# Optimization experiments

Measured on AMD Instinct MI355X. Metric: run time of the kernel, lower is better.

## Reference

```python
import jax, jax.numpy as jnp
import numpy as np

EMBED, HEADS, LEVELS, POINTS = 256, 8, 1, 4


def setup_inputs():
    key = jax.random.key(0)
    ks = jax.random.split(key, 8)
    B, NQ = 8, 8192
    Hh, Ww = 128, 128
    E, Hn, L, P = EMBED, HEADS, LEVELS, POINTS
    s = 1.0 / np.sqrt(E)
    return dict(
        query=jax.random.normal(ks[0], (B, NQ, E), jnp.float32),
        value=jax.random.normal(ks[1], (B, Hh * Ww, E), jnp.float32),
        ref_2d=jax.random.uniform(ks[2], (B, NQ, L, 2), dtype=jnp.float32),
        spatial_shapes=jnp.array([[Hh, Ww]], dtype=jnp.int32),
        W_off=jax.random.normal(ks[3], (E, Hn * L * P * 2), jnp.float32) * 0.01,
        b_off=jax.random.normal(ks[4], (Hn * L * P * 2,), jnp.float32) * 0.5,
        W_attn=jax.random.normal(ks[5], (E, Hn * L * P), jnp.float32) * s,
        b_attn=jnp.zeros((Hn * L * P,), jnp.float32),
        W_val=jax.random.normal(ks[6], (E, E), jnp.float32) * s,
        b_val=jnp.zeros((E,), jnp.float32),
        W_out=jax.random.normal(ks[7], (E, E), jnp.float32) * s,
        b_out=jnp.zeros((E,), jnp.float32),
    )


def _bilinear_sample(v, loc, Hl, Wl):
    # v: (B, Hn, Hl*Wl, dh); loc: (B, Hn, NQ, P, 2) normalized [0,1] (x, y)
    B, Hn, NQ, P, _ = loc.shape
    dh = v.shape[-1]
    # torch grid_sample(align_corners=False) pixel coords: p = loc * size - 0.5
    x = loc[..., 0] * Wl - 0.5
    y = loc[..., 1] * Hl - 0.5
    x0 = jnp.floor(x); y0 = jnp.floor(y)
    x1 = x0 + 1.0; y1 = y0 + 1.0
    wx1 = x - x0; wx0 = 1.0 - wx1
    wy1 = y - y0; wy0 = 1.0 - wy1

    def corner(xc, yc, w):
        valid = (xc >= 0) & (xc < Wl) & (yc >= 0) & (yc < Hl)  # zeros padding
        xi = jnp.clip(xc, 0, Wl - 1).astype(jnp.int32)
        yi = jnp.clip(yc, 0, Hl - 1).astype(jnp.int32)
        idx = (yi * Wl + xi).reshape(B, Hn, NQ * P, 1)
        vals = jnp.take_along_axis(v, idx, axis=2).reshape(B, Hn, NQ, P, dh)
        return vals * (w * valid.astype(v.dtype))[..., None]

    return (corner(x0, y0, wx0 * wy0) + corner(x1, y0, wx1 * wy0)
            + corner(x0, y1, wx0 * wy1) + corner(x1, y1, wx1 * wy1))


def _forward(query, value, ref_2d, W_off, b_off, W_attn, b_attn, W_val, b_val, W_out, b_out, shapes):
    B, NQ, E = query.shape
    Hn, L, P = HEADS, LEVELS, POINTS
    dh = E // Hn
    NV = value.shape[1]
    identity = query
    v = (value @ W_val + b_val).reshape(B, NV, Hn, dh)
    off = (query @ W_off + b_off).reshape(B, NQ, Hn, L, P, 2)
    attn = jax.nn.softmax((query @ W_attn + b_attn).reshape(B, NQ, Hn, L * P), axis=-1)
    attn = attn.reshape(B, NQ, Hn, L, P)
    # offset_normalizer = (W, H) per level
    norm = jnp.asarray(shapes[:, ::-1].copy(), dtype=query.dtype)
    loc = ref_2d[:, :, None, :, None, :] + off / norm[None, None, None, :, None, :]
    loc = jnp.transpose(loc, (0, 2, 1, 3, 4, 5))   # (B, Hn, NQ, L, P, 2)
    attn_t = jnp.transpose(attn, (0, 2, 1, 3, 4))  # (B, Hn, NQ, L, P)
    v_t = jnp.transpose(v, (0, 2, 1, 3))           # (B, Hn, NV, dh)
    starts = np.concatenate([[0], np.cumsum(shapes[:, 0] * shapes[:, 1])]).astype(np.int64)
    out = jnp.zeros((B, Hn, NQ, dh), query.dtype)
    for l in range(L):  # static small loop over feature levels
        Hl, Wl = int(shapes[l, 0]), int(shapes[l, 1])
        v_l = v_t[:, :, int(starts[l]):int(starts[l + 1]), :]
        samp = _bilinear_sample(v_l, loc[:, :, :, l], Hl, Wl)  # (B,Hn,NQ,P,dh)
        out = out + jnp.sum(samp * attn_t[:, :, :, l, :, None], axis=3)
    out = jnp.transpose(out, (0, 2, 1, 3)).reshape(B, NQ, E)
    # dropout is identity at eval time
    return out @ W_out + b_out + identity


def reference(query, value, ref_2d, spatial_shapes, W_off, b_off, W_attn, b_attn, W_val, b_val, W_out, b_out):
    shapes = np.asarray(jax.device_get(spatial_shapes))  # static level shapes
    return _forward(query, value, ref_2d, W_off, b_off, W_attn, b_attn, W_val, b_val, W_out, b_out, shapes)
```

## Files before the change

### kernel.cpp

```cpp
#include <hip/hip_runtime.h>

typedef short s16x8 __attribute__((ext_vector_type(8)));
typedef float f32x4 __attribute__((ext_vector_type(4)));

#define HN 8
#define PP 4
#define DH 32
#define NQc 8192
#define NVc 16384
#define EE 256
#define HWc 128

__device__ __forceinline__ unsigned short f2bf(float x) {
  unsigned u = __float_as_uint(x);
  u += 0x7FFF + ((u >> 16) & 1);
  return (unsigned short)(u >> 16);
}
__device__ __forceinline__ float bf2f(unsigned short h) {
  return __uint_as_float(((unsigned)h) << 16);
}

__global__ __launch_bounds__(256) void wprep(
    const float* __restrict__ Wval, const float* __restrict__ Wout,
    const float* __restrict__ Woff, const float* __restrict__ Wattn,
    const float* __restrict__ boff, const float* __restrict__ battn,
    unsigned short* __restrict__ wvt, unsigned short* __restrict__ wot,
    unsigned short* __restrict__ wct, float* __restrict__ bcat) {
  int g = blockIdx.x * 256 + threadIdx.x;
  if (g < 65536) {
    int n = g >> 8, k = g & 255;
    wvt[n * 256 + k] = f2bf(Wval[k * 256 + n]);
  } else if (g < 131072) {
    int g2 = g - 65536;
    int n = g2 >> 8, k = g2 & 255;
    wot[n * 256 + k] = f2bf(Wout[k * 256 + n]);
  } else if (g < 163840) {
    int g2 = g - 131072;
    int n = g2 >> 8, k = g2 & 255;
    float v = 0.f;
    if (n < 64) v = Woff[k * 64 + n];
    else if (n < 96) v = Wattn[k * 32 + (n - 64)];
    wct[n * 256 + k] = f2bf(v);
  } else if (g < 163968) {
    int c = g - 163840;
    bcat[c] = (c < 64) ? boff[c] : ((c < 96) ? battn[c - 64] : 0.f);
  }
}

#define MODE_VAL 0
#define MODE_PLAIN 1
#define MODE_OUT 2

template <int MODE>
struct SmemBytes { static constexpr int v = 20480; };
template <> struct SmemBytes<MODE_PLAIN> { static constexpr int v = 51200; };

template <int MODE, bool ABF16>
__global__ __launch_bounds__(256) void mfma_gemm(
    const void* __restrict__ Ain, const unsigned short* __restrict__ Wt,
    const float* __restrict__ bias, const float* __restrict__ resid,
    const float* __restrict__ ref2d, unsigned int* __restrict__ meta,
    void* __restrict__ outp) {
  __shared__ __align__(16) char smem[SmemBytes<MODE>::v];
  unsigned short* As = (unsigned short*)smem;
  unsigned short* Ws = As + 128 * 40;
  const int t = threadIdx.x;
  const int lane = t & 63, wave = t >> 6;
  const int lane15 = lane & 15, quad = lane >> 4;
  const int wr = wave >> 1, wc = wave & 1;
  const int bm = blockIdx.x * 128, bn = blockIdx.y * 128;

  f32x4 acc[4][4];
#pragma unroll
  for (int i = 0; i < 4; ++i)
#pragma unroll
    for (int j = 0; j < 4; ++j)
#pragma unroll
      for (int r = 0; r < 4; ++r) acc[i][j][r] = 0.f;

  const int ar = t >> 3, ac = (t & 7) * 4;
  const int wr2 = t >> 1, wcp = (t & 1) * 2;

  float4 av[4];
  uint4 ab0, ab1, wv0, wv1;

#define LOAD_TILE(K0)                                                          \
  do {                                                                         \
    if (!ABF16) {                                                              \
      const float* Af = (const float*)Ain;                                     \
      _Pragma("unroll") for (int i = 0; i < 4; ++i)                            \
          av[i] = *(const float4*)(Af + (size_t)(bm + ar + i * 32) * 256 +     \
                                   (K0) + ac);                                 \
    } else {                                                                   \
      const unsigned short* Ab = (const unsigned short*)Ain;                   \
      ab0 = *(const uint4*)(Ab + (size_t)(bm + wr2) * 256 + (K0) + wcp * 8);   \
      ab1 = *(const uint4*)(Ab + (size_t)(bm + wr2) * 256 + (K0) + wcp * 8 + 8); \
    }                                                                          \
    wv0 = *(const uint4*)(Wt + (size_t)(bn + wr2) * 256 + (K0) + wcp * 8);     \
    wv1 = *(const uint4*)(Wt + (size_t)(bn + wr2) * 256 + (K0) + wcp * 8 + 8); \
  } while (0)

  LOAD_TILE(0);

  for (int k0 = 0; k0 < 256; k0 += 32) {
    __syncthreads();
    if (!ABF16) {
#pragma unroll
      for (int i = 0; i < 4; ++i) {
        ushort4 c;
        c.x = f2bf(av[i].x); c.y = f2bf(av[i].y); c.z = f2bf(av[i].z); c.w = f2bf(av[i].w);
        *(ushort4*)&As[(ar + i * 32) * 40 + ac] = c;
      }
    } else {
      *(uint4*)&As[wr2 * 40 + wcp * 8] = ab0;
      *(uint4*)&As[wr2 * 40 + wcp * 8 + 8] = ab1;
    }
    *(uint4*)&Ws[wr2 * 40 + wcp * 8] = wv0;
    *(uint4*)&Ws[wr2 * 40 + wcp * 8 + 8] = wv1;
    __syncthreads();
    if (k0 < 224) LOAD_TILE(k0 + 32);
    s16x8 af[4], bfr[4];
#pragma unroll
    for (int tm = 0; tm < 4; ++tm)
      af[tm] = *(const s16x8*)&As[(wr * 64 + tm * 16 + lane15) * 40 + quad * 8];
#pragma unroll
    for (int tn = 0; tn < 4; ++tn)
      bfr[tn] = *(const s16x8*)&Ws[(wc * 64 + tn * 16 + lane15) * 40 + quad * 8];
#pragma unroll
    for (int tm = 0; tm < 4; ++tm)
#pragma unroll
      for (int tn = 0; tn < 4; ++tn)
        acc[tm][tn] = __builtin_amdgcn_mfma_f32_16x16x32_bf16(bfr[tn], af[tm], acc[tm][tn], 0, 0, 0);
  }
#undef LOAD_TILE

  if (MODE == MODE_VAL) {
    unsigned short* outs = (unsigned short*)outp;
    const size_t b = (size_t)(bm >> 14);
    const int n0 = bm & (NVc - 1);
#pragma unroll
    for (int tn = 0; tn < 4; ++tn) {
      const int ch0 = bn + wc * 64 + tn * 16 + quad * 4;
      const float4 b4 = *(const float4*)&bias[ch0];
      const int h = ch0 >> 5, dh0 = ch0 & 31;
#pragma unroll
      for (int tm = 0; tm < 4; ++tm) {
        const int n = n0 + wr * 64 + tm * 16 + lane15;
        ushort4 o;
        o.x = f2bf(acc[tm][tn][0] + b4.x);
        o.y = f2bf(acc[tm][tn][1] + b4.y);
        o.z = f2bf(acc[tm][tn][2] + b4.z);
        o.w = f2bf(acc[tm][tn][3] + b4.w);
        *(ushort4*)(outs + ((b * HN + h) * NVc + n) * DH + dh0) = o;
      }
    }
  } else if (MODE == MODE_PLAIN) {
    float* Cf = (float*)smem;
    __syncthreads();
#pragma unroll
    for (int tn = 0; tn < 4; ++tn) {
      const int col0 = wc * 64 + tn * 16 + quad * 4;
      if (col0 < 96) {
        const float4 b4 = *(const float4*)&bias[col0];
#pragma unroll
        for (int tm = 0; tm < 4; ++tm) {
          const int m = wr * 64 + tm * 16 + lane15;
          float4 v;
          v.x = acc[tm][tn][0] + b4.x;
          v.y = acc[tm][tn][1] + b4.y;
          v.z = acc[tm][tn][2] + b4.z;
          v.w = acc[tm][tn][3] + b4.w;
          *(float4*)&Cf[m * 100 + col0] = v;
        }
      }
    }
    __syncthreads();
#pragma unroll
    for (int i = 0; i < 4; ++i) {
      const int task = i * 256 + t;
      const int h = task & 7, rowl = task >> 3;
      const int bq = bm + rowl;
      const float* row = Cf + rowl * 100;
      const float rx = ref2d[(size_t)bq * 2 + 0];
      const float ry = ref2d[(size_t)bq * 2 + 1];
      const float l0 = row[64 + h * 4 + 0], l1 = row[64 + h * 4 + 1];
      const float l2 = row[64 + h * 4 + 2], l3 = row[64 + h * 4 + 3];
      const float mx = fmaxf(fmaxf(l0, l1), fmaxf(l2, l3));
      float e0 = __expf(l0 - mx), e1 = __expf(l1 - mx), e2 = __expf(l2 - mx), e3 = __expf(l3 - mx);
      const float inv = 1.0f / (e0 + e1 + e2 + e3);
      float ee[4] = {e0, e1, e2, e3};
      unsigned int* m = meta + ((size_t)bq * 8 + h) * 20;
      uint4 pk;
      float4 wts[4];
#pragma unroll
      for (int p = 0; p < PP; ++p) {
        const float a = ee[p] * inv;
        const float ox = row[h * 8 + p * 2 + 0];
        const float oy = row[h * 8 + p * 2 + 1];
        const float x = (rx + ox * (1.0f / HWc)) * (float)HWc - 0.5f;
        const float y = (ry + oy * (1.0f / HWc)) * (float)HWc - 0.5f;
        const float x0f = floorf(x), y0f = floorf(y);
        const int x0 = (int)x0f, y0 = (int)y0f;
        const float wx1 = x - x0f, wx0 = 1.f - wx1;
        const float wy1 = y - y0f, wy0 = 1.f - wy1;
        const bool vx0 = (unsigned)x0 < (unsigned)HWc, vx1 = (unsigned)(x0 + 1) < (unsigned)HWc;
        const bool vy0 = (unsigned)y0 < (unsigned)HWc, vy1 = (unsigned)(y0 + 1) < (unsigned)HWc;
        const int xi0 = min(max(x0, 0), HWc - 1), xi1 = min(max(x0 + 1, 0), HWc - 1);
        const int yi0 = min(max(y0, 0), HWc - 1), yi1 = min(max(y0 + 1, 0), HWc - 1);
        const unsigned pv = (unsigned)xi0 | ((unsigned)yi0 << 8) | ((unsigned)xi1 << 16) | ((unsigned)yi1 << 24);
        if (p == 0) pk.x = pv; else if (p == 1) pk.y = pv; else if (p == 2) pk.z = pv; else pk.w = pv;
        float4 w;
        w.x = (vx0 && vy0) ? a * wx0 * wy0 : 0.f;
        w.y = (vx1 && vy0) ? a * wx1 * wy0 : 0.f;
        w.z = (vx0 && vy1) ? a * wx0 * wy1 : 0.f;
        w.w = (vx1 && vy1) ? a * wx1 * wy1 : 0.f;
        wts[p] = w;
      }
      *(uint4*)m = pk;
#pragma unroll
      for (int p = 0; p < PP; ++p) *(float4*)&m[4 + p * 4] = wts[p];
    }
  } else {
    float* outf = (float*)outp;
#pragma unroll
    for (int tn = 0; tn < 4; ++tn) {
      const int ch0 = bn + wc * 64 + tn * 16 + quad * 4;
      const float4 b4 = *(const float4*)&bias[ch0];
#pragma unroll
      for (int tm = 0; tm < 4; ++tm) {
        const size_t row = (size_t)bm + wr * 64 + tm * 16 + lane15;
        float4 rs = *(const float4*)(resid + row * 256 + ch0);
        float4 v;
        v.x = acc[tm][tn][0] + b4.x + rs.x;
        v.y = acc[tm][tn][1] + b4.y + rs.y;
        v.z = acc[tm][tn][2] + b4.z + rs.z;
        v.w = acc[tm][tn][3] + b4.w + rs.w;
        *(float4*)(outf + row * 256 + ch0) = v;
      }
    }
  }
}

__global__ __launch_bounds__(256) void sample_kernel(
    const unsigned short* __restrict__ vbuf,
    const unsigned int* __restrict__ meta,
    unsigned short* __restrict__ outs) {
  const int t = threadIdx.x;
  const int d4 = (t & 7) << 2;
  const int ql = t >> 3;
  const int sl = blockIdx.x >> 8;
  const int qc = blockIdx.x & 255;
  const int b = sl >> 3;
  const int h = sl & 7;
  const int q = qc * 32 + ql;
  const size_t bq = (size_t)b * NQc + q;
  const unsigned int* m = meta + ((size_t)bq * 8 + h) * 20;
  const uint4 pk = *(const uint4*)m;
  const unsigned short* vb = vbuf + (size_t)sl * (NVc * DH) + d4;

  float4 acc = {0.f, 0.f, 0.f, 0.f};
#pragma unroll
  for (int p = 0; p < PP; ++p) {
    const unsigned P = (p == 0) ? pk.x : (p == 1) ? pk.y : (p == 2) ? pk.z : pk.w;
    const float4 w = *(const float4*)(m + 4 + p * 4);
    const int x0 = P & 255, y0 = (P >> 8) & 255, x1 = (P >> 16) & 255, y1 = P >> 24;
    const int r0 = y0 << 12, r1 = y1 << 12;
    const ushort4 v00 = *(const ushort4*)(vb + r0 + (x0 << 5));
    const ushort4 v10 = *(const ushort4*)(vb + r0 + (x1 << 5));
    const ushort4 v01 = *(const ushort4*)(vb + r1 + (x0 << 5));
    const ushort4 v11 = *(const ushort4*)(vb + r1 + (x1 << 5));
    acc.x += w.x * bf2f(v00.x); acc.y += w.x * bf2f(v00.y);
    acc.z += w.x * bf2f(v00.z); acc.w += w.x * bf2f(v00.w);
    acc.x += w.y * bf2f(v10.x); acc.y += w.y * bf2f(v10.y);
    acc.z += w.y * bf2f(v10.z); acc.w += w.y * bf2f(v10.w);
    acc.x += w.z * bf2f(v01.x); acc.y += w.z * bf2f(v01.y);
    acc.z += w.z * bf2f(v01.z); acc.w += w.z * bf2f(v01.w);
    acc.x += w.w * bf2f(v11.x); acc.y += w.w * bf2f(v11.y);
    acc.z += w.w * bf2f(v11.z); acc.w += w.w * bf2f(v11.w);
  }
  ushort4 o;
  o.x = f2bf(acc.x); o.y = f2bf(acc.y); o.z = f2bf(acc.z); o.w = f2bf(acc.w);
  *(ushort4*)(outs + bq * EE + h * DH + d4) = o;
}

extern "C" void kernel_launch(void* const* d_in, const int* in_sizes, int n_in,
                              void* d_out, int out_size, void* d_ws, size_t ws_size,
                              hipStream_t stream) {
  const float* query = (const float*)d_in[0];
  const float* value = (const float*)d_in[1];
  const float* ref2d = (const float*)d_in[2];
  const float* Woff  = (const float*)d_in[4];
  const float* boff  = (const float*)d_in[5];
  const float* Wattn = (const float*)d_in[6];
  const float* battn = (const float*)d_in[7];
  const float* Wval  = (const float*)d_in[8];
  const float* bval  = (const float*)d_in[9];
  const float* Wout  = (const float*)d_in[10];
  const float* bout  = (const float*)d_in[11];
  float* out = (float*)d_out;

  unsigned short* vbuf = (unsigned short*)d_ws;
  unsigned int* meta   = (unsigned int*)(vbuf + 33554432);
  unsigned short* sbuf = (unsigned short*)(meta + 10485760);
  unsigned short* wvt  = sbuf + 16777216;
  unsigned short* wot  = wvt + 65536;
  unsigned short* wct  = wot + 65536;
  float* bcat          = (float*)(wct + 32768);

  wprep<<<641, 256, 0, stream>>>(Wval, Wout, Woff, Wattn, boff, battn, wvt, wot, wct, bcat);

  mfma_gemm<MODE_VAL, false><<<dim3(1024, 2), 256, 0, stream>>>(
      (const void*)value, wvt, bval, nullptr, nullptr, nullptr, (void*)vbuf);

  mfma_gemm<MODE_PLAIN, false><<<dim3(512, 1), 256, 0, stream>>>(
      (const void*)query, wct, bcat, nullptr, ref2d, meta, nullptr);

  sample_kernel<<<16384, 256, 0, stream>>>(vbuf, meta, sbuf);

  mfma_gemm<MODE_OUT, true><<<dim3(512, 2), 256, 0, stream>>>(
      (const void*)sbuf, wot, bout, query, nullptr, nullptr, (void*)out);
}
```

Measured before the change: 424.0 us.

## Double-buffer GEMM shared-memory tiles and coalesce output epilogue through LDS

The GEMM main loop now uses two shared-memory tile buffers, so each iteration needs one barrier instead of two and the next tile's LDS store overlaps with the current tile's MFMA work. The fp32 output epilogue (MODE_OUT/PLAIN) now stages accumulators through LDS in two half-tile passes, giving row-contiguous, coalesced residual reads and output writes. This doubles LDS use for the VAL/OUT variants, which may lower occupancy, and adds extra barriers in the epilogue.

Result: no change. 426.0 us (+0.5%).

```diff
diff --git a/kernel.cpp b/kernel.cpp
--- a/kernel.cpp
+++ b/kernel.cpp
@@ -52,7 +52,7 @@
 #define MODE_OUT 2
 
 template <int MODE>
-struct SmemBytes { static constexpr int v = 20480; };
+struct SmemBytes { static constexpr int v = 40960; };
 template <> struct SmemBytes<MODE_PLAIN> { static constexpr int v = 51200; };
 
 template <int MODE, bool ABF16>
@@ -62,8 +62,10 @@
     const float* __restrict__ ref2d, unsigned int* __restrict__ meta,
     void* __restrict__ outp) {
   __shared__ __align__(16) char smem[SmemBytes<MODE>::v];
-  unsigned short* As = (unsigned short*)smem;
-  unsigned short* Ws = As + 128 * 40;
+  unsigned short* As0 = (unsigned short*)smem;
+  unsigned short* Ws0 = As0 + 128 * 40;
+  unsigned short* As1 = Ws0 + 128 * 40;
+  unsigned short* Ws1 = As1 + 128 * 40;
   const int t = threadIdx.x;
   const int lane = t & 63, wave = t >> 6;
   const int lane15 = lane & 15, quad = lane >> 4;
@@ -100,39 +102,53 @@
     wv1 = *(const uint4*)(Wt + (size_t)(bn + wr2) * 256 + (K0) + wcp * 8 + 8); \
   } while (0)
 
+#define STAGE(AsD, WsD)                                                        \
+  do {                                                                         \
+    if (!ABF16) {                                                              \
+      _Pragma("unroll") for (int i = 0; i < 4; ++i) {                          \
+        ushort4 c;                                                             \
+        c.x = f2bf(av[i].x); c.y = f2bf(av[i].y);                              \
+        c.z = f2bf(av[i].z); c.w = f2bf(av[i].w);                              \
+        *(ushort4*)&(AsD)[(ar + i * 32) * 40 + ac] = c;                        \
+      }                                                                        \
+    } else {                                                                   \
+      *(uint4*)&(AsD)[wr2 * 40 + wcp * 8] = ab0;                               \
+      *(uint4*)&(AsD)[wr2 * 40 + wcp * 8 + 8] = ab1;                           \
+    }                                                                          \
+    *(uint4*)&(WsD)[wr2 * 40 + wcp * 8] = wv0;                                 \
+    *(uint4*)&(WsD)[wr2 * 40 + wcp * 8 + 8] = wv1;                             \
+  } while (0)
+
   LOAD_TILE(0);
-
-  for (int k0 = 0; k0 < 256; k0 += 32) {
-    __syncthreads();
-    if (!ABF16) {
-#pragma unroll
-      for (int i = 0; i < 4; ++i) {
-        ushort4 c;
-        c.x = f2bf(av[i].x); c.y = f2bf(av[i].y); c.z = f2bf(av[i].z); c.w = f2bf(av[i].w);
-        *(ushort4*)&As[(ar + i * 32) * 40 + ac] = c;
-      }
-    } else {
-      *(uint4*)&As[wr2 * 40 + wcp * 8] = ab0;
-      *(uint4*)&As[wr2 * 40 + wcp * 8 + 8] = ab1;
-    }
-    *(uint4*)&Ws[wr2 * 40 + wcp * 8] = wv0;
-    *(uint4*)&Ws[wr2 * 40 + wcp * 8 + 8] = wv1;
-    __syncthreads();
-    if (k0 < 224) LOAD_TILE(k0 + 32);
+  STAGE(As0, Ws0);
+  __syncthreads();
+
+#pragma unroll
+  for (int kk = 0; kk < 8; ++kk) {
+    unsigned short* Ar = (kk & 1) ? As1 : As0;
+    unsigned short* Wr = (kk & 1) ? Ws1 : Ws0;
+    if (kk < 7) LOAD_TILE((kk + 1) * 32);
     s16x8 af[4], bfr[4];
 #pragma unroll
     for (int tm = 0; tm < 4; ++tm)
-      af[tm] = *(const s16x8*)&As[(wr * 64 + tm * 16 + lane15) * 40 + quad * 8];
+      af[tm] = *(const s16x8*)&Ar[(wr * 64 + tm * 16 + lane15) * 40 + quad * 8];
 #pragma unroll
     for (int tn = 0; tn < 4; ++tn)
-      bfr[tn] = *(const s16x8*)&Ws[(wc * 64 + tn * 16 + lane15) * 40 + quad * 8];
+      bfr[tn] = *(const s16x8*)&Wr[(wc * 64 + tn * 16 + lane15) * 40 + quad * 8];
 #pragma unroll
     for (int tm = 0; tm < 4; ++tm)
 #pragma unroll
       for (int tn = 0; tn < 4; ++tn)
         acc[tm][tn] = __builtin_amdgcn_mfma_f32_16x16x32_bf16(bfr[tn], af[tm], acc[tm][tn], 0, 0, 0);
+    if (kk < 7) {
+      unsigned short* Aw = (kk & 1) ? As0 : As1;
+      unsigned short* Ww = (kk & 1) ? Ws0 : Ws1;
+      STAGE(Aw, Ww);
+      __syncthreads();
+    }
   }
 #undef LOAD_TILE
+#undef STAGE
 
   if (MODE == MODE_VAL) {
     unsigned short* outs = (unsigned short*)outp;
@@ -221,21 +237,38 @@
       for (int p = 0; p < PP; ++p) *(float4*)&m[4 + p * 4] = wts[p];
     }
   } else {
+    float* Cf = (float*)smem;
     float* outf = (float*)outp;
 #pragma unroll
-    for (int tn = 0; tn < 4; ++tn) {
-      const int ch0 = bn + wc * 64 + tn * 16 + quad * 4;
-      const float4 b4 = *(const float4*)&bias[ch0];
-#pragma unroll
-      for (int tm = 0; tm < 4; ++tm) {
-        const size_t row = (size_t)bm + wr * 64 + tm * 16 + lane15;
-        float4 rs = *(const float4*)(resid + row * 256 + ch0);
-        float4 v;
-        v.x = acc[tm][tn][0] + b4.x + rs.x;
-        v.y = acc[tm][tn][1] + b4.y + rs.y;
-        v.z = acc[tm][tn][2] + b4.z + rs.z;
-        v.w = acc[tm][tn][3] + b4.w + rs.w;
-        *(float4*)(outf + row * 256 + ch0) = v;
+    for (int pass = 0; pass < 2; ++pass) {
+      __syncthreads();
+      if (wr == pass) {
+#pragma unroll
+        for (int tn = 0; tn < 4; ++tn) {
+          const int col0 = wc * 64 + tn * 16 + quad * 4;
+          const float4 b4 = *(const float4*)&bias[bn + col0];
+#pragma unroll
+          for (int tm = 0; tm < 4; ++tm) {
+            const int rowl = tm * 16 + lane15;
+            float4 v;
+            v.x = acc[tm][tn][0] + b4.x;
+            v.y = acc[tm][tn][1] + b4.y;
+            v.z = acc[tm][tn][2] + b4.z;
+            v.w = acc[tm][tn][3] + b4.w;
+            *(float4*)&Cf[rowl * 132 + col0] = v;
+          }
+        }
+      }
+      __syncthreads();
+#pragma unroll
+      for (int i = 0; i < 8; ++i) {
+        const int id = i * 256 + t;
+        const int n = id >> 5, c = id & 31;
+        const size_t row = (size_t)bm + pass * 64 + n;
+        float4 v = *(const float4*)&Cf[n * 132 + c * 4];
+        float4 rs = *(const float4*)(resid + row * 256 + bn + c * 4);
+        v.x += rs.x; v.y += rs.y; v.z += rs.z; v.w += rs.w;
+        *(float4*)(outf + row * 256 + bn + c * 4) = v;
       }
     }
   }
```

## Stage output GEMM epilogue through LDS and remap sample-kernel block order

Applied to the files above, without the earlier changes.

The output-projection GEMM epilogue now writes bias-added accumulators into padded shared memory in two half-tile passes. It then reads them back so each thread issues fully coalesced row-contiguous float4 loads of the residual and stores of the output. This replaces the scattered per-lane-row stores and raises the kernel's shared memory to about 33 KB, with extra barriers. Separately, the sampling kernel's block index is remapped so consecutive blocks cycle across 8 heads/slices for the same query chunk. This is meant to improve cache locality or spread of the value-buffer gathers.

After: 418.4 us. Within noise of the previous version (-1.3%).

```diff
diff --git a/kernel.cpp b/kernel.cpp
--- a/kernel.cpp
+++ b/kernel.cpp
@@ -54,6 +54,7 @@
 template <int MODE>
 struct SmemBytes { static constexpr int v = 20480; };
 template <> struct SmemBytes<MODE_PLAIN> { static constexpr int v = 51200; };
+template <> struct SmemBytes<MODE_OUT>   { static constexpr int v = 33792; };
 
 template <int MODE, bool ABF16>
 __global__ __launch_bounds__(256) void mfma_gemm(
@@ -221,21 +222,38 @@
       for (int p = 0; p < PP; ++p) *(float4*)&m[4 + p * 4] = wts[p];
     }
   } else {
+    float* Cf = (float*)smem;
     float* outf = (float*)outp;
 #pragma unroll
-    for (int tn = 0; tn < 4; ++tn) {
-      const int ch0 = bn + wc * 64 + tn * 16 + quad * 4;
-      const float4 b4 = *(const float4*)&bias[ch0];
-#pragma unroll
-      for (int tm = 0; tm < 4; ++tm) {
-        const size_t row = (size_t)bm + wr * 64 + tm * 16 + lane15;
-        float4 rs = *(const float4*)(resid + row * 256 + ch0);
-        float4 v;
-        v.x = acc[tm][tn][0] + b4.x + rs.x;
-        v.y = acc[tm][tn][1] + b4.y + rs.y;
-        v.z = acc[tm][tn][2] + b4.z + rs.z;
-        v.w = acc[tm][tn][3] + b4.w + rs.w;
-        *(float4*)(outf + row * 256 + ch0) = v;
+    for (int pass = 0; pass < 2; ++pass) {
+      __syncthreads();
+      if (wr == pass) {
+#pragma unroll
+        for (int tn = 0; tn < 4; ++tn) {
+          const int col0 = wc * 64 + tn * 16 + quad * 4;
+          const float4 b4 = *(const float4*)&bias[bn + col0];
+#pragma unroll
+          for (int tm = 0; tm < 4; ++tm) {
+            const int rowl = tm * 16 + lane15;
+            float4 v;
+            v.x = acc[tm][tn][0] + b4.x;
+            v.y = acc[tm][tn][1] + b4.y;
+            v.z = acc[tm][tn][2] + b4.z;
+            v.w = acc[tm][tn][3] + b4.w;
+            *(float4*)&Cf[rowl * 132 + col0] = v;
+          }
+        }
+      }
+      __syncthreads();
+#pragma unroll
+      for (int i = 0; i < 8; ++i) {
+        const int id = i * 256 + t;
+        const int n = id >> 5, c = id & 31;
+        const size_t row = (size_t)bm + pass * 64 + n;
+        float4 v = *(const float4*)&Cf[n * 132 + c * 4];
+        float4 rs = *(const float4*)(resid + row * 256 + bn + c * 4);
+        v.x += rs.x; v.y += rs.y; v.z += rs.z; v.w += rs.w;
+        *(float4*)(outf + row * 256 + bn + c * 4) = v;
       }
     }
   }
@@ -248,8 +266,13 @@
   const int t = threadIdx.x;
   const int d4 = (t & 7) << 2;
   const int ql = t >> 3;
-  const int sl = blockIdx.x >> 8;
-  const int qc = blockIdx.x & 255;
+  const int j = blockIdx.x;
+  const int x = j & 7;
+  const int s = j >> 3;
+  const int m_ = s & 255;
+  const int gi = s >> 8;
+  const int sl = x + 8 * gi;
+  const int qc = m_;
   const int b = sl >> 3;
   const int h = sl & 7;
   const int q = qc * 32 + ql;
```
